# Performance work log

Measured on AMD Instinct MI355X. Metric: run time of the kernel, lower is better.

Reference implementation:

```python
import jax, jax.numpy as jnp
import numpy as np

B, P, V, M = 4, 4, 4096, 2048
BIG = 1e10  # masking constant for invalid points in min-reductions


def setup_inputs() -> dict:
    key = jax.random.key(0)
    k1, k2, k3, k4, k5 = jax.random.split(key, 5)
    vertices = jax.random.normal(k1, (B, V, 3), jnp.float32)
    # 3x4 projection matrices; force the 3rd row so w = 0.05*z + 4 > 0 (no divide blowup)
    projmats = 0.5 * jax.random.normal(k2, (P, 3, 4), jnp.float32)
    projmats = projmats.at[:, 2, :].set(jnp.array([0.0, 0.0, 0.05, 4.0], jnp.float32))
    edgemaps = jax.random.normal(k3, (B, P, M, 2), jnp.float32)
    boundary_mask = jax.random.bernoulli(k4, 0.3, (B, P, V))
    edgemaps_len = jax.random.randint(k5, (B, P), M // 2, M + 1, jnp.int32)
    return {"vertices": vertices, "projmats": projmats, "edgemaps": edgemaps,
            "boundary_mask": boundary_mask, "edgemaps_len": edgemaps_len}


def reference(vertices, projmats, edgemaps, boundary_mask, edgemaps_len):
    # --- project vertices into all views (homogeneous + perspective divide) ---
    ones = jnp.ones(vertices.shape[:2] + (1,), vertices.dtype)
    vh = jnp.concatenate([vertices, ones], axis=-1)              # (B,V,4)
    proj = jnp.einsum('pij,bvj->bpvi', projmats, vh)             # (B,P,V,3)
    pts = proj[..., :2] / proj[..., 2:3]                         # (B,P,V,2)

    # --- masked pairwise squared distances (GEMM-form, no (.,.,2) broadcast) ---
    x2 = jnp.sum(pts * pts, axis=-1)                             # (B,P,V)
    y2 = jnp.sum(edgemaps * edgemaps, axis=-1)                   # (B,P,M)
    xy = jnp.einsum('bpvc,bpmc->bpvm', pts, edgemaps)            # (B,P,V,M)
    d2 = jnp.maximum(x2[..., :, None] + y2[..., None, :] - 2.0 * xy, 0.0)

    xmask = boundary_mask.astype(d2.dtype)                       # (B,P,V)
    ymask = (jnp.arange(M)[None, None, :] < edgemaps_len[..., None]).astype(d2.dtype)

    # min over valid targets / valid boundary points
    cham_x = jnp.min(jnp.where(ymask[:, :, None, :] > 0, d2, BIG), axis=-1)  # (B,P,V)
    cham_y = jnp.min(jnp.where(xmask[:, :, :, None] > 0, d2, BIG), axis=-2)  # (B,P,M)

    x_len = jnp.maximum(jnp.sum(xmask, axis=-1), 1.0)            # (B,P)
    y_len = jnp.maximum(jnp.sum(ymask, axis=-1), 1.0)            # (B,P)
    loss_p = jnp.sum(xmask * cham_x, -1) / x_len + jnp.sum(ymask * cham_y, -1) / y_len
    return jnp.mean(loss_p, axis=-1)                             # (B,) per-mesh chamfer loss
```

## Files before the change

### kernel.cpp

```cpp
#include <hip/hip_runtime.h>
#include <stdint.h>

namespace {
constexpr int B = 4, P = 4, V = 4096, M = 2048;
constexpr int BP = B * P;
constexpr float BIGF = 1e10f;
constexpr int TPB   = 256;
constexpr int OTILE = 128;
constexpr int XT = V / OTILE;
constexpr int YT = M / OTILE;
constexpr int ROLES = XT + YT;
constexpr int CH = 512;
constexpr int KPB = 8;
constexpr int VPB = V / KPB;
constexpr int MPB = M / KPB;
}


__global__ __launch_bounds__(256) void prep_kernel(
    const float* __restrict__ vertices,
    const float* __restrict__ projmats,
    const uint8_t* __restrict__ maskraw,
    const float* __restrict__ edgemaps,
    int* __restrict__ nvalid,
    float* __restrict__ sx,
    float* __restrict__ sy,
    int* __restrict__ done,
    int* __restrict__ done2,
    float4* __restrict__ pnk,
    float4* __restrict__ epk)
{
    const int bp = blockIdx.x / KPB;
    const int k  = blockIdx.x % KPB;
    const int b = bp / P, p = bp % P;
    const int tid = threadIdx.x;
    const int lane = tid & 63;
    const int wave = tid >> 6;

    __shared__ int s_res[4];
    __shared__ int s_cnt;
    __shared__ int s_prew[4];
    if (tid < 4) { s_res[tid] = 0; s_prew[tid] = 0; }
    if (tid == 0) s_cnt = 0;
    __syncthreads();

    uint32_t loc[4] = {0u, 0u, 0u, 0u};
    const int NB = 16384;
    for (int i = tid * 16; i < NB; i += 256 * 16) {
        const uint32_t* w = (const uint32_t*)(maskraw + i);
        const uint32_t orw = w[0] | w[1] | w[2] | w[3];
        loc[0] |= orw & 0x000000FFu;
        loc[1] |= orw & 0x0000FF00u;
        loc[2] |= orw & 0x00FF0000u;
        loc[3] |= orw & 0xFF000000u;
    }
    #pragma unroll
    for (int j = 0; j < 4; ++j)
        if (loc[j]) atomicOr(&s_res[j], 1);
    __syncthreads();
    int layout;
    if (!s_res[1] && !s_res[2] && !s_res[3]) layout = 1;
    else if (!s_res[0] && !s_res[1])         layout = 2;
    else                                      layout = 0;

    {
        const float2* eg = (const float2*)edgemaps + (size_t)bp * M;
        for (int m = k * MPB + tid; m < (k + 1) * MPB; m += 256) {
            const float2 e = eg[m];
            epk[(size_t)bp * M + m] =
                make_float4(e.x, e.y, fmaf(e.x, e.x, e.y * e.y), 0.f);
        }
    }

    const int pre_n = k * VPB;
    int cnt = 0;
    if (layout == 0) {
        const uint8_t* mk = maskraw + (size_t)bp * V;
        for (int i = tid; i < pre_n; i += 256) cnt += (mk[i] != 0);
    } else if (layout == 1) {
        const int* mk = (const int*)maskraw + (size_t)bp * V;
        for (int i = tid; i < pre_n; i += 256) cnt += (mk[i] != 0);
    } else {
        const float* mk = (const float*)maskraw + (size_t)bp * V;
        for (int i = tid; i < pre_n; i += 256) cnt += (mk[i] != 0.0f);
    }
    #pragma unroll
    for (int off = 32; off > 0; off >>= 1) cnt += __shfl_down(cnt, off, 64);
    if (lane == 0) s_prew[wave] = cnt;
    __syncthreads();
    const int pre_total = s_prew[0] + s_prew[1] + s_prew[2] + s_prew[3];

    float mm[12];
    #pragma unroll
    for (int j = 0; j < 12; ++j) mm[j] = projmats[p * 12 + j];

    for (int v = k * VPB + tid; v < (k + 1) * VPB; v += 256) {
        const int mi = bp * V + v;
        bool msk;
        if (layout == 0)      msk = maskraw[mi] != 0;
        else if (layout == 1) msk = ((const int*)maskraw)[mi] != 0;
        else                  msk = ((const float*)maskraw)[mi] != 0.0f;

        const unsigned long long ball = __ballot(msk);
        const int bcnt = __popcll(ball);
        int base = 0;
        if (lane == 0 && bcnt) base = atomicAdd(&s_cnt, bcnt);
        base = __shfl(base, 0, 64);
        if (msk) {
            const float x = vertices[(b * V + v) * 3 + 0];
            const float y = vertices[(b * V + v) * 3 + 1];
            const float z = vertices[(b * V + v) * 3 + 2];
            const float u  = mm[0]*x + mm[1]*y + mm[2]*z  + mm[3];
            const float vv = mm[4]*x + mm[5]*y + mm[6]*z  + mm[7];
            const float w  = mm[8]*x + mm[9]*y + mm[10]*z + mm[11];
            const int off = __popcll(ball & ((1ull << lane) - 1ull));
            const float rw = 1.0f / w;
            const float px = u * rw, py = vv * rw;
            pnk[(size_t)bp * V + pre_total + base + off] =
                make_float4(px, py, fmaf(px, px, py * py), 0.f);
        }
    }
    __syncthreads();
    if (tid == 0) {
        if (k == KPB - 1) nvalid[bp] = pre_total + s_cnt;
        if (k == 0) { sx[bp] = 0.0f; sy[bp] = 0.0f; done[bp] = 0; }
        if (blockIdx.x == 0) *done2 = 0;
    }
}

__global__ __launch_bounds__(TPB) void chamfer_kernel(
    const int* __restrict__ elen,
    int* __restrict__ nvalid,
    float* __restrict__ sx,
    float* __restrict__ sy,
    int* __restrict__ done,
    int* __restrict__ done2,
    const float4* __restrict__ pnk,
    const float4* __restrict__ epk,
    float* __restrict__ out)
{
    const int bp   = blockIdx.x;
    const int role = blockIdx.y;
    const int tid  = threadIdx.x;
    const int wave = tid >> 6;
    const int lane = tid & 63;
    const int len  = elen[bp];
    const int nv   = nvalid[bp];

    __shared__ float4 sb[4][CH];
    __shared__ float  smin[4][OTILE];
    __shared__ int    s_last;

    const float4* outer; const float4* inner;
    int lim, L, obase;
    float* acc;
    const bool isY = (role < YT);
    if (isY) {
        obase = role * OTILE;
        outer = epk + (size_t)bp * M;  lim = len;
        inner = pnk + (size_t)bp * V;  L = nv;
        acc = &sy[bp];
    } else {
        obase = (role - YT) * OTILE;
        outer = pnk + (size_t)bp * V;  lim = nv;
        inner = epk + (size_t)bp * M;  L = len;
        acc = &sx[bp];
    }
    const bool active = (obase < lim);

    float pn0 = 0.f, pn1 = 0.f;
    if (active) {
        const float4 p0 = outer[obase + lane];
        const float4 p1 = outer[obase + 64 + lane];
        const float a0 = -2.0f * p0.x, b0 = -2.0f * p0.y;  pn0 = p0.z;
        const float a1 = -2.0f * p1.x, b1 = -2.0f * p1.y;  pn1 = p1.z;

        const int q = (L + 3) >> 2;
        const int is = wave * q;
        const int ie = min(is + q, L);
        float4* sbw = sb[wave];

        float mn0 = BIGF, mn1 = BIGF;
        for (int cs = is; cs < ie; cs += CH) {
            const int cnt  = min(CH, ie - cs);
            const int cnt8 = (cnt + 7) & ~7;
            for (int j = lane; j < cnt; j += 64) sbw[j] = inner[cs + j];
            for (int j = cnt + lane; j < cnt8; j += 64)
                sbw[j] = make_float4(0.f, 0.f, BIGF, 0.f);
            #pragma unroll 8
            for (int j = 0; j < cnt8; ++j) {
                const float4 t = sbw[j];
                mn0 = fminf(mn0, fmaf(t.x, a0, fmaf(t.y, b0, t.z)));
                mn1 = fminf(mn1, fmaf(t.x, a1, fmaf(t.y, b1, t.z)));
            }
        }
        smin[wave][lane]      = mn0;
        smin[wave][64 + lane] = mn1;
    }
    __syncthreads();
    if (active && wave == 0) {
        const float m0 = fminf(fminf(smin[0][lane],      smin[1][lane]),
                               fminf(smin[2][lane],      smin[3][lane]));
        const float m1 = fminf(fminf(smin[0][64 + lane], smin[1][64 + lane]),
                               fminf(smin[2][64 + lane], smin[3][64 + lane]));
        float val = 0.0f;
        if (obase + lane < lim)      val += fmaxf(m0 + pn0, 0.0f);
        if (obase + 64 + lane < lim) val += fmaxf(m1 + pn1, 0.0f);
        #pragma unroll
        for (int off = 32; off > 0; off >>= 1)
            val += __shfl_down(val, off, 64);
        if (lane == 0) atomicAdd(acc, val);
    }

    __syncthreads();
    if (tid == 0) {
        __threadfence();
        int lastall = 0;
        const int old = atomicAdd(&done[bp], 1);
        if (old == ROLES - 1) {
            __threadfence();
            const int o2 = atomicAdd(done2, 1);
            lastall = (o2 == BP - 1) ? 1 : 0;
        }
        s_last = lastall;
    }
    __syncthreads();
    if (s_last) {
        __threadfence();
        if (tid < B) {
            float o = 0.0f;
            #pragma unroll
            for (int p = 0; p < P; ++p) {
                const int j = tid * P + p;
                o += sx[j] / fmaxf((float)nvalid[j], 1.0f)
                   + sy[j] / fmaxf((float)elen[j], 1.0f);
            }
            out[tid] = o * (1.0f / P);
        }
    }
}

extern "C" void kernel_launch(void* const* d_in, const int* in_sizes, int n_in,
                              void* d_out, int out_size, void* d_ws, size_t ws_size,
                              hipStream_t stream)
{
    const float*   vertices = (const float*)d_in[0];
    const float*   projmats = (const float*)d_in[1];
    const float*   edgemaps = (const float*)d_in[2];
    const uint8_t* maskraw  = (const uint8_t*)d_in[3];
    const int*     elen     = (const int*)d_in[4];
    float* out = (float*)d_out;

    char* ws = (char*)d_ws;
    int*    nvalid = (int*)(ws + 0);
    float*  sx     = (float*)(ws + 64);
    float*  sy     = (float*)(ws + 128);
    int*    done   = (int*)(ws + 192);
    int*    done2  = (int*)(ws + 256);
    float4* pnk    = (float4*)(ws + 512);
    float4* epk    = pnk + (size_t)BP * V;

    prep_kernel<<<BP * KPB, 256, 0, stream>>>(vertices, projmats, maskraw,
                                              edgemaps, nvalid, sx, sy, done,
                                              done2, pnk, epk);
    chamfer_kernel<<<dim3(BP, ROLES), TPB, 0, stream>>>(elen, nvalid, sx, sy,
                                                        done, done2, pnk, epk,
                                                        out);
}
```

Measured before the change: 92.77 us.

## Fuse prep and chamfer kernels into one persistent kernel with flag-based dependencies

Merges the projection/packing kernel and the chamfer reduction kernel into a single persistent-style launch of 512 blocks that loop over work items. Chamfer items spin-wait on per-prep-block salted flags instead of relying on a kernel boundary. Completion detection changes from a global counter to per-bp salted flags, so the workspace no longer needs resetting between calls. Also doubles the number of prep splits per (b,p). This removes one launch and the inter-kernel gap, but adds spin-wait overhead and depends on prep items being scheduled before the chamfer items that wait on them.

```diff
diff --git a/kernel.cpp b/kernel.cpp
--- a/kernel.cpp
+++ b/kernel.cpp
@@ -11,231 +11,259 @@
 constexpr int YT = M / OTILE;
 constexpr int ROLES = XT + YT;
 constexpr int CH = 512;
-constexpr int KPB = 8;
+constexpr int KPB = 16;
 constexpr int VPB = V / KPB;
 constexpr int MPB = M / KPB;
-}
-
-
-__global__ __launch_bounds__(256) void prep_kernel(
+constexpr int NPREP  = BP * KPB;
+constexpr int NCH    = BP * ROLES;
+constexpr int NITEMS = NPREP + NCH;
+constexpr int GRID   = 512;
+}
+
+__device__ __forceinline__ int psalt(int i) {
+    return (int)(0x9E3779B9u ^ ((unsigned)i * 0x01000193u));
+}
+__device__ __forceinline__ int csalt(int i) {
+    return (int)(0xC001D00Du ^ ((unsigned)i * 0x85EBCA6Bu));
+}
+
+
+__global__ __launch_bounds__(TPB, 2) void fused_kernel(
     const float* __restrict__ vertices,
     const float* __restrict__ projmats,
     const uint8_t* __restrict__ maskraw,
     const float* __restrict__ edgemaps,
-    int* __restrict__ nvalid,
-    float* __restrict__ sx,
-    float* __restrict__ sy,
-    int* __restrict__ done,
-    int* __restrict__ done2,
-    float4* __restrict__ pnk,
-    float4* __restrict__ epk)
-{
-    const int bp = blockIdx.x / KPB;
-    const int k  = blockIdx.x % KPB;
-    const int b = bp / P, p = bp % P;
-    const int tid = threadIdx.x;
-    const int lane = tid & 63;
-    const int wave = tid >> 6;
-
-    __shared__ int s_res[4];
-    __shared__ int s_cnt;
-    __shared__ int s_prew[4];
-    if (tid < 4) { s_res[tid] = 0; s_prew[tid] = 0; }
-    if (tid == 0) s_cnt = 0;
-    __syncthreads();
-
-    uint32_t loc[4] = {0u, 0u, 0u, 0u};
-    const int NB = 16384;
-    for (int i = tid * 16; i < NB; i += 256 * 16) {
-        const uint32_t* w = (const uint32_t*)(maskraw + i);
-        const uint32_t orw = w[0] | w[1] | w[2] | w[3];
-        loc[0] |= orw & 0x000000FFu;
-        loc[1] |= orw & 0x0000FF00u;
-        loc[2] |= orw & 0x00FF0000u;
-        loc[3] |= orw & 0xFF000000u;
-    }
-    #pragma unroll
-    for (int j = 0; j < 4; ++j)
-        if (loc[j]) atomicOr(&s_res[j], 1);
-    __syncthreads();
-    int layout;
-    if (!s_res[1] && !s_res[2] && !s_res[3]) layout = 1;
-    else if (!s_res[0] && !s_res[1])         layout = 2;
-    else                                      layout = 0;
-
-    {
-        const float2* eg = (const float2*)edgemaps + (size_t)bp * M;
-        for (int m = k * MPB + tid; m < (k + 1) * MPB; m += 256) {
-            const float2 e = eg[m];
-            epk[(size_t)bp * M + m] =
-                make_float4(e.x, e.y, fmaf(e.x, e.x, e.y * e.y), 0.f);
-        }
-    }
-
-    const int pre_n = k * VPB;
-    int cnt = 0;
-    if (layout == 0) {
-        const uint8_t* mk = maskraw + (size_t)bp * V;
-        for (int i = tid; i < pre_n; i += 256) cnt += (mk[i] != 0);
-    } else if (layout == 1) {
-        const int* mk = (const int*)maskraw + (size_t)bp * V;
-        for (int i = tid; i < pre_n; i += 256) cnt += (mk[i] != 0);
-    } else {
-        const float* mk = (const float*)maskraw + (size_t)bp * V;
-        for (int i = tid; i < pre_n; i += 256) cnt += (mk[i] != 0.0f);
-    }
-    #pragma unroll
-    for (int off = 32; off > 0; off >>= 1) cnt += __shfl_down(cnt, off, 64);
-    if (lane == 0) s_prew[wave] = cnt;
-    __syncthreads();
-    const int pre_total = s_prew[0] + s_prew[1] + s_prew[2] + s_prew[3];
-
-    float mm[12];
-    #pragma unroll
-    for (int j = 0; j < 12; ++j) mm[j] = projmats[p * 12 + j];
-
-    for (int v = k * VPB + tid; v < (k + 1) * VPB; v += 256) {
-        const int mi = bp * V + v;
-        bool msk;
-        if (layout == 0)      msk = maskraw[mi] != 0;
-        else if (layout == 1) msk = ((const int*)maskraw)[mi] != 0;
-        else                  msk = ((const float*)maskraw)[mi] != 0.0f;
-
-        const unsigned long long ball = __ballot(msk);
-        const int bcnt = __popcll(ball);
-        int base = 0;
-        if (lane == 0 && bcnt) base = atomicAdd(&s_cnt, bcnt);
-        base = __shfl(base, 0, 64);
-        if (msk) {
-            const float x = vertices[(b * V + v) * 3 + 0];
-            const float y = vertices[(b * V + v) * 3 + 1];
-            const float z = vertices[(b * V + v) * 3 + 2];
-            const float u  = mm[0]*x + mm[1]*y + mm[2]*z  + mm[3];
-            const float vv = mm[4]*x + mm[5]*y + mm[6]*z  + mm[7];
-            const float w  = mm[8]*x + mm[9]*y + mm[10]*z + mm[11];
-            const int off = __popcll(ball & ((1ull << lane) - 1ull));
-            const float rw = 1.0f / w;
-            const float px = u * rw, py = vv * rw;
-            pnk[(size_t)bp * V + pre_total + base + off] =
-                make_float4(px, py, fmaf(px, px, py * py), 0.f);
-        }
-    }
-    __syncthreads();
-    if (tid == 0) {
-        if (k == KPB - 1) nvalid[bp] = pre_total + s_cnt;
-        if (k == 0) { sx[bp] = 0.0f; sy[bp] = 0.0f; done[bp] = 0; }
-        if (blockIdx.x == 0) *done2 = 0;
-    }
-}
-
-__global__ __launch_bounds__(TPB) void chamfer_kernel(
     const int* __restrict__ elen,
     int* __restrict__ nvalid,
     float* __restrict__ sx,
     float* __restrict__ sy,
     int* __restrict__ done,
-    int* __restrict__ done2,
-    const float4* __restrict__ pnk,
-    const float4* __restrict__ epk,
+    int* __restrict__ pflag,
+    int* __restrict__ cflag,
+    float4* __restrict__ pnk,
+    float4* __restrict__ epk,
     float* __restrict__ out)
 {
-    const int bp   = blockIdx.x;
-    const int role = blockIdx.y;
     const int tid  = threadIdx.x;
+    const int lane = tid & 63;
     const int wave = tid >> 6;
-    const int lane = tid & 63;
-    const int len  = elen[bp];
-    const int nv   = nvalid[bp];
 
     __shared__ float4 sb[4][CH];
     __shared__ float  smin[4][OTILE];
-    __shared__ int    s_last;
-
-    const float4* outer; const float4* inner;
-    int lim, L, obase;
-    float* acc;
-    const bool isY = (role < YT);
-    if (isY) {
-        obase = role * OTILE;
-        outer = epk + (size_t)bp * M;  lim = len;
-        inner = pnk + (size_t)bp * V;  L = nv;
-        acc = &sy[bp];
-    } else {
-        obase = (role - YT) * OTILE;
-        outer = pnk + (size_t)bp * V;  lim = nv;
-        inner = epk + (size_t)bp * M;  L = len;
-        acc = &sx[bp];
-    }
-    const bool active = (obase < lim);
-
-    float pn0 = 0.f, pn1 = 0.f;
-    if (active) {
-        const float4 p0 = outer[obase + lane];
-        const float4 p1 = outer[obase + 64 + lane];
-        const float a0 = -2.0f * p0.x, b0 = -2.0f * p0.y;  pn0 = p0.z;
-        const float a1 = -2.0f * p1.x, b1 = -2.0f * p1.y;  pn1 = p1.z;
-
-        const int q = (L + 3) >> 2;
-        const int is = wave * q;
-        const int ie = min(is + q, L);
-        float4* sbw = sb[wave];
-
-        float mn0 = BIGF, mn1 = BIGF;
-        for (int cs = is; cs < ie; cs += CH) {
-            const int cnt  = min(CH, ie - cs);
-            const int cnt8 = (cnt + 7) & ~7;
-            for (int j = lane; j < cnt; j += 64) sbw[j] = inner[cs + j];
-            for (int j = cnt + lane; j < cnt8; j += 64)
-                sbw[j] = make_float4(0.f, 0.f, BIGF, 0.f);
-            #pragma unroll 8
-            for (int j = 0; j < cnt8; ++j) {
-                const float4 t = sbw[j];
-                mn0 = fminf(mn0, fmaf(t.x, a0, fmaf(t.y, b0, t.z)));
-                mn1 = fminf(mn1, fmaf(t.x, a1, fmaf(t.y, b1, t.z)));
-            }
-        }
-        smin[wave][lane]      = mn0;
-        smin[wave][64 + lane] = mn1;
-    }
-    __syncthreads();
-    if (active && wave == 0) {
-        const float m0 = fminf(fminf(smin[0][lane],      smin[1][lane]),
-                               fminf(smin[2][lane],      smin[3][lane]));
-        const float m1 = fminf(fminf(smin[0][64 + lane], smin[1][64 + lane]),
-                               fminf(smin[2][64 + lane], smin[3][64 + lane]));
-        float val = 0.0f;
-        if (obase + lane < lim)      val += fmaxf(m0 + pn0, 0.0f);
-        if (obase + 64 + lane < lim) val += fmaxf(m1 + pn1, 0.0f);
-        #pragma unroll
-        for (int off = 32; off > 0; off >>= 1)
-            val += __shfl_down(val, off, 64);
-        if (lane == 0) atomicAdd(acc, val);
-    }
-
-    __syncthreads();
-    if (tid == 0) {
-        __threadfence();
-        int lastall = 0;
-        const int old = atomicAdd(&done[bp], 1);
-        if (old == ROLES - 1) {
+    __shared__ int    s_misc[10];
+
+    for (int item = blockIdx.x; item < NITEMS; item += gridDim.x) {
+        __syncthreads();
+
+        if (item < NPREP) {
+            const int bp = item / KPB;
+            const int k  = item % KPB;
+            const int b = bp / P, p = bp % P;
+
+            if (tid < 4) { s_misc[tid] = 0; s_misc[5 + tid] = 0; }
+            if (tid == 0) {
+                s_misc[4] = 0;
+                if (k == 0) {
+                    sx[bp] = 0.0f; sy[bp] = 0.0f; done[bp] = 0;
+                }
+            }
+            __syncthreads();
+
+            uint32_t loc[4] = {0u, 0u, 0u, 0u};
+            const int NB = 16384;
+            for (int i = tid * 16; i < NB; i += 256 * 16) {
+                const uint32_t* w = (const uint32_t*)(maskraw + i);
+                const uint32_t orw = w[0] | w[1] | w[2] | w[3];
+                loc[0] |= orw & 0x000000FFu;
+                loc[1] |= orw & 0x0000FF00u;
+                loc[2] |= orw & 0x00FF0000u;
+                loc[3] |= orw & 0xFF000000u;
+            }
+            #pragma unroll
+            for (int j = 0; j < 4; ++j)
+                if (loc[j]) atomicOr(&s_misc[j], 1);
+            __syncthreads();
+            int layout;
+            if (!s_misc[1] && !s_misc[2] && !s_misc[3]) layout = 1;
+            else if (!s_misc[0] && !s_misc[1])          layout = 2;
+            else                                         layout = 0;
+
+            {
+                const float2* eg = (const float2*)edgemaps + (size_t)bp * M;
+                for (int m = k * MPB + tid; m < (k + 1) * MPB; m += 256) {
+                    const float2 e = eg[m];
+                    epk[(size_t)bp * M + m] =
+                        make_float4(e.x, e.y, fmaf(e.x, e.x, e.y * e.y), 0.f);
+                }
+            }
+
+            const int pre_n = k * VPB;
+            int cnt = 0;
+            if (layout == 0) {
+                const uint8_t* mk = maskraw + (size_t)bp * V;
+                for (int i = tid; i < pre_n; i += 256) cnt += (mk[i] != 0);
+            } else if (layout == 1) {
+                const int* mk = (const int*)maskraw + (size_t)bp * V;
+                for (int i = tid; i < pre_n; i += 256) cnt += (mk[i] != 0);
+            } else {
+                const float* mk = (const float*)maskraw + (size_t)bp * V;
+                for (int i = tid; i < pre_n; i += 256) cnt += (mk[i] != 0.0f);
+            }
+            #pragma unroll
+            for (int off = 32; off > 0; off >>= 1)
+                cnt += __shfl_down(cnt, off, 64);
+            if (lane == 0) s_misc[5 + wave] = cnt;
+            __syncthreads();
+            const int pre_total =
+                s_misc[5] + s_misc[6] + s_misc[7] + s_misc[8];
+
+            float mm[12];
+            #pragma unroll
+            for (int j = 0; j < 12; ++j) mm[j] = projmats[p * 12 + j];
+
+            for (int v = k * VPB + tid; v < (k + 1) * VPB; v += 256) {
+                const int mi = bp * V + v;
+                bool msk;
+                if (layout == 0)      msk = maskraw[mi] != 0;
+                else if (layout == 1) msk = ((const int*)maskraw)[mi] != 0;
+                else                  msk = ((const float*)maskraw)[mi] != 0.0f;
+
+                const unsigned long long ball = __ballot(msk);
+                const int bcnt = __popcll(ball);
+                int base = 0;
+                if (lane == 0 && bcnt) base = atomicAdd(&s_misc[4], bcnt);
+                base = __shfl(base, 0, 64);
+                if (msk) {
+                    const float x = vertices[(b * V + v) * 3 + 0];
+                    const float y = vertices[(b * V + v) * 3 + 1];
+                    const float z = vertices[(b * V + v) * 3 + 2];
+                    const float u  = mm[0]*x + mm[1]*y + mm[2]*z  + mm[3];
+                    const float vv = mm[4]*x + mm[5]*y + mm[6]*z  + mm[7];
+                    const float w  = mm[8]*x + mm[9]*y + mm[10]*z + mm[11];
+                    const int off = __popcll(ball & ((1ull << lane) - 1ull));
+                    const float rw = 1.0f / w;
+                    const float px = u * rw, py = vv * rw;
+                    pnk[(size_t)bp * V + pre_total + base + off] =
+                        make_float4(px, py, fmaf(px, px, py * py), 0.f);
+                }
+            }
+            __syncthreads();
+            if (tid == 0) {
+                if (k == KPB - 1) nvalid[bp] = pre_total + s_misc[4];
+                __threadfence();
+                atomicExch(&pflag[item * 16], psalt(item));
+            }
+        } else {
+            const int c    = item - NPREP;
+            const int bp   = c % BP;
+            const int rr   = c / BP;
+            const int len  = elen[bp];
+
+            if (wave == 0) {
+                const int fi  = bp * KPB + (lane & 15);
+                const int ex  = psalt(fi);
+                for (;;) {
+                    bool ok = true;
+                    if (lane < KPB)
+                        ok = (atomicAdd(&pflag[fi * 16], 0) == ex);
+                    if (__all(ok)) break;
+                    __builtin_amdgcn_s_sleep(8);
+                }
+            }
+            __syncthreads();
             __threadfence();
-            const int o2 = atomicAdd(done2, 1);
-            lastall = (o2 == BP - 1) ? 1 : 0;
-        }
-        s_last = lastall;
-    }
-    __syncthreads();
-    if (s_last) {
-        __threadfence();
-        if (tid < B) {
-            float o = 0.0f;
-            #pragma unroll
-            for (int p = 0; p < P; ++p) {
-                const int j = tid * P + p;
-                o += sx[j] / fmaxf((float)nvalid[j], 1.0f)
-                   + sy[j] / fmaxf((float)elen[j], 1.0f);
-            }
-            out[tid] = o * (1.0f / P);
+            const int nv = nvalid[bp];
+
+            const float4* outer; const float4* inner;
+            int lim, L, obase;
+            float* acc;
+            if (rr < YT) {
+                obase = rr * OTILE;
+                outer = epk + (size_t)bp * M;  lim = len;
+                inner = pnk + (size_t)bp * V;  L = nv;
+                acc = &sy[bp];
+            } else {
+                obase = (rr - YT) * OTILE;
+                outer = pnk + (size_t)bp * V;  lim = nv;
+                inner = epk + (size_t)bp * M;  L = len;
+                acc = &sx[bp];
+            }
+            const bool active = (obase < lim);
+
+            float pn0 = 0.f, pn1 = 0.f;
+            if (active) {
+                const float4 p0 = outer[obase + lane];
+                const float4 p1 = outer[obase + 64 + lane];
+                const float a0 = -2.0f * p0.x, b0 = -2.0f * p0.y;  pn0 = p0.z;
+                const float a1 = -2.0f * p1.x, b1 = -2.0f * p1.y;  pn1 = p1.z;
+
+                const int q  = (L + 3) >> 2;
+                const int is = wave * q;
+                const int ie = min(is + q, L);
+                float4* sbw = sb[wave];
+
+                float mn0 = BIGF, mn1 = BIGF;
+                for (int cs = is; cs < ie; cs += CH) {
+                    const int cnt  = min(CH, ie - cs);
+                    const int cnt8 = (cnt + 7) & ~7;
+                    for (int j = lane; j < cnt; j += 64) sbw[j] = inner[cs + j];
+                    for (int j = cnt + lane; j < cnt8; j += 64)
+                        sbw[j] = make_float4(0.f, 0.f, BIGF, 0.f);
+                    #pragma unroll 8
+                    for (int j = 0; j < cnt8; ++j) {
+                        const float4 t = sbw[j];
+                        mn0 = fminf(mn0, fmaf(t.x, a0, fmaf(t.y, b0, t.z)));
+                        mn1 = fminf(mn1, fmaf(t.x, a1, fmaf(t.y, b1, t.z)));
+                    }
+                }
+                smin[wave][lane]      = mn0;
+                smin[wave][64 + lane] = mn1;
+            }
+            __syncthreads();
+            if (active && wave == 0) {
+                const float m0 = fminf(fminf(smin[0][lane],    smin[1][lane]),
+                                       fminf(smin[2][lane],    smin[3][lane]));
+                const float m1 = fminf(fminf(smin[0][64+lane], smin[1][64+lane]),
+                                       fminf(smin[2][64+lane], smin[3][64+lane]));
+                float val = 0.0f;
+                if (obase + lane < lim)      val += fmaxf(m0 + pn0, 0.0f);
+                if (obase + 64 + lane < lim) val += fmaxf(m1 + pn1, 0.0f);
+                #pragma unroll
+                for (int off = 32; off > 0; off >>= 1)
+                    val += __shfl_down(val, off, 64);
+                if (lane == 0) atomicAdd(acc, val);
+            }
+
+            __syncthreads();
+            if (tid == 0) {
+                __threadfence();
+                int lastall = 0;
+                const int old = atomicAdd(&done[bp], 1);
+                if (old == ROLES - 1) {
+                    __threadfence();
+                    atomicExch(&cflag[bp * 16], csalt(bp));
+                    lastall = 1;
+                    for (int j = 0; j < BP; ++j)
+                        if (atomicAdd(&cflag[j * 16], 0) != csalt(j)) {
+                            lastall = 0; break;
+                        }
+                }
+                s_misc[9] = lastall;
+            }
+            __syncthreads();
+            if (s_misc[9]) {
+                __threadfence();
+                if (tid < B) {
+                    float o = 0.0f;
+                    #pragma unroll
+                    for (int p = 0; p < P; ++p) {
+                        const int j = tid * P + p;
+                        o += sx[j] / fmaxf((float)nvalid[j], 1.0f)
+                           + sy[j] / fmaxf((float)elen[j], 1.0f);
+                    }
+                    out[tid] = o * (1.0f / P);
+                }
+            }
         }
     }
 }
@@ -256,14 +284,12 @@
     float*  sx     = (float*)(ws + 64);
     float*  sy     = (float*)(ws + 128);
     int*    done   = (int*)(ws + 192);
-    int*    done2  = (int*)(ws + 256);
-    float4* pnk    = (float4*)(ws + 512);
+    int*    pflag  = (int*)(ws + 512);
+    int*    cflag  = (int*)(ws + 16896);
+    float4* pnk    = (float4*)(ws + 32768);
     float4* epk    = pnk + (size_t)BP * V;
 
-    prep_kernel<<<BP * KPB, 256, 0, stream>>>(vertices, projmats, maskraw,
-                                              edgemaps, nvalid, sx, sy, done,
-                                              done2, pnk, epk);
-    chamfer_kernel<<<dim3(BP, ROLES), TPB, 0, stream>>>(elen, nvalid, sx, sy,
-                                                        done, done2, pnk, epk,
-                                                        out);
-}
+    fused_kernel<<<GRID, TPB, 0, stream>>>(vertices, projmats, maskraw,
+                                           edgemaps, elen, nvalid, sx, sy,
+                                           done, pflag, cflag, pnk, epk, out);
+}
```

After: 141.4 us. 1.52x slower.
